# Kernel optimization log

Measured on AMD Instinct MI355X. Metric: run time of the kernel, lower is better.

## Reference

```python
import jax, jax.numpy as jnp
import numpy as np

N_NODES = 100000


def _gcn_layer(h, W, b, src, dst, norm, n):
    # h: [N, Fin] -> transform then normalized scatter-add aggregation
    h = h @ W                                   # [N, Fout]
    msg = h[src] * norm[:, None]                # [E', Fout] gather + scale
    out = jax.ops.segment_sum(msg, dst, num_segments=n)  # scatter-add
    return out + b


def setup_inputs() -> dict:
    key = jax.random.key(0)
    k1, k2, k3, k4 = jax.random.split(key, 4)
    N, F_IN, HID, C, E = N_NODES, 512, 128, 40, 1600000
    x = jax.random.normal(k1, (N, F_IN), dtype=jnp.float32)
    edge_index = jax.random.randint(k2, (2, E), 0, N, dtype=jnp.int64)
    W1 = jax.random.normal(k3, (F_IN, HID), dtype=jnp.float32) * (1.0 / np.sqrt(F_IN))
    b1 = jnp.zeros((HID,), dtype=jnp.float32)
    W2 = jax.random.normal(k4, (HID, C), dtype=jnp.float32) * (1.0 / np.sqrt(HID))
    b2 = jnp.zeros((C,), dtype=jnp.float32)
    return {"x": x, "edge_index": edge_index, "W1": W1, "b1": b1, "W2": W2, "b2": b2}


def reference(x, edge_index, W1, b1, W2, b2):
    n = x.shape[0]
    # add self-loops (GCNConv default)
    loop = jnp.arange(n, dtype=edge_index.dtype)
    src = jnp.concatenate([edge_index[0], loop])
    dst = jnp.concatenate([edge_index[1], loop])
    # symmetric normalization: deg counted on destination (in-degree, incl. self-loop)
    deg = jax.ops.segment_sum(jnp.ones_like(dst, dtype=x.dtype), dst, num_segments=n)
    dis = jnp.where(deg > 0, jax.lax.rsqrt(deg), 0.0)  # deg^{-1/2}
    norm = dis[src] * dis[dst]                          # per-edge weight

    h = jax.nn.relu(_gcn_layer(x, W1, b1, src, dst, norm, n))
    # dropout: identity in eval mode (training=False)
    h = _gcn_layer(h, W2, b2, src, dst, norm, n)
    return jax.nn.log_softmax(h, axis=1)
```

## Files before the change

### kernel.cpp

```cpp
#include <hip/hip_runtime.h>
#include <hip/hip_bf16.h>


#define F_IN 512
#define HID  128
#define NC   40

typedef __attribute__((ext_vector_type(8))) short bf16x8;
typedef __attribute__((ext_vector_type(4))) float f32x4v;

__device__ __forceinline__ ushort f2bf(float f) {
    union { float f; unsigned u; } x; x.f = f;
    unsigned r = x.u + 0x7FFFu + ((x.u >> 16) & 1u);
    return (ushort)(r >> 16);
}
__device__ __forceinline__ float bf2f(ushort u) {
    return __uint_as_float((unsigned)u << 16);
}
__device__ __forceinline__ bf16x8 cvt8(float4 lo, float4 hi) {
    __align__(16) ushort t[8];
    t[0]=f2bf(lo.x); t[1]=f2bf(lo.y); t[2]=f2bf(lo.z); t[3]=f2bf(lo.w);
    t[4]=f2bf(hi.x); t[5]=f2bf(hi.y); t[6]=f2bf(hi.z); t[7]=f2bf(hi.w);
    return *(const bf16x8*)t;
}

__global__ void count_deg(const int* __restrict__ dst, int E, unsigned* __restrict__ cnt) {
    int t = blockIdx.x * blockDim.x + threadIdx.x;
    if (t < E) atomicAdd(&cnt[dst[t]], 1u);
}

__global__ __launch_bounds__(1024) void scan_block(const unsigned* __restrict__ cnt,
                                                   unsigned* __restrict__ offs,
                                                   unsigned* __restrict__ bsums,
                                                   float* __restrict__ dis, int N) {
    __shared__ unsigned s[1024];
    int tid = threadIdx.x;
    int i = blockIdx.x * 1024 + tid;
    unsigned v = (i < N) ? cnt[i] : 0u;
    if (i < N) dis[i] = rsqrtf((float)v + 1.0f);
    s[tid] = v;
    __syncthreads();
    #pragma unroll
    for (int d = 1; d < 1024; d <<= 1) {
        unsigned t = (tid >= d) ? s[tid - d] : 0u;
        __syncthreads();
        s[tid] += t;
        __syncthreads();
    }
    if (i < N) offs[i] = s[tid] - v;
    if (tid == 1023) bsums[blockIdx.x] = s[1023];
}

__global__ __launch_bounds__(1024) void scan_bsums(unsigned* __restrict__ bsums, int nb) {
    __shared__ unsigned s[1024];
    int tid = threadIdx.x;
    unsigned v = (tid < nb) ? bsums[tid] : 0u;
    s[tid] = v;
    __syncthreads();
    #pragma unroll
    for (int d = 1; d < 1024; d <<= 1) {
        unsigned t = (tid >= d) ? s[tid - d] : 0u;
        __syncthreads();
        s[tid] += t;
        __syncthreads();
    }
    if (tid < nb) bsums[tid] = s[tid] - v;
}

__global__ __launch_bounds__(1024) void scan_add(unsigned* __restrict__ offs,
                                                 const unsigned* __restrict__ bsums,
                                                 int N, unsigned total) {
    int i = blockIdx.x * 1024 + threadIdx.x;
    if (i < N) offs[i] += bsums[blockIdx.x];
    if (i == 0) offs[N] = total;
}

__global__ void fill_csr(const int* __restrict__ src, const int* __restrict__ dst,
                         const unsigned* __restrict__ offs, unsigned* __restrict__ cursor,
                         int* __restrict__ col, int E) {
    int t = blockIdx.x * blockDim.x + threadIdx.x;
    if (t >= E) return;
    int s = src[t], d = dst[t];
    unsigned pos = offs[d] + atomicAdd(&cursor[d], 1u);
    col[pos] = s;
}

__global__ void packW(const float* __restrict__ W1, const float* __restrict__ W2,
                      ushort* __restrict__ W1p, ushort* __restrict__ W2p) {
    int t = blockIdx.x * 256 + threadIdx.x;
    if (t < 65536) {
        int j = t & 7, n = (t >> 3) & 127, kb = (t >> 10) & 3, s = t >> 12;
        int k = s * 32 + kb * 8 + j;
        W1p[t] = f2bf(W1[(size_t)k * HID + n]);
    } else {
        int q = t - 65536;
        if (q < 6144) {
            int j = q & 7;
            int i2 = q >> 3;
            int n = i2 % 48;
            int i3 = i2 / 48;
            int kb = i3 & 3, ks = i3 >> 2;
            int k = ks * 32 + kb * 8 + j;
            float v = (n < NC) ? W2[(size_t)k * NC + n] : 0.f;
            W2p[q] = f2bf(v);
        }
    }
}

__global__ __launch_bounds__(256) void gemm1_mfma(const float* __restrict__ A,
                                                  const ushort* __restrict__ Bp,
                                                  const float* __restrict__ dis,
                                                  ushort* __restrict__ C, int N) {
    const int tid  = threadIdx.x;
    const int wave = tid >> 6;
    const int lane = tid & 63;
    const int quad = lane >> 4;
    const int mr   = lane & 15;
    const int base = (blockIdx.x * 4 + wave) * 32;
    if (base >= N) return;
    const int r0 = base + mr;
    const int r1 = base + 16 + mr;
    const bool ok0 = r0 < N, ok1 = r1 < N;
    const float* ap0 = A + (size_t)(ok0 ? r0 : 0) * F_IN + quad * 8;
    const float* ap1 = A + (size_t)(ok1 ? r1 : 0) * F_IN + quad * 8;
    const ushort* bp = Bp + quad * 1024 + mr * 8;

    f32x4v acc0[8], acc1[8];
    #pragma unroll
    for (int t = 0; t < 8; t++) {
        acc0[t] = (f32x4v){0.f, 0.f, 0.f, 0.f};
        acc1[t] = (f32x4v){0.f, 0.f, 0.f, 0.f};
    }

    float4 av[2][4];
    #pragma unroll
    for (int b = 0; b < 2; b++) {
        av[b][0] = *(const float4*)(ap0 + b * 32);
        av[b][1] = *(const float4*)(ap0 + b * 32 + 4);
        av[b][2] = *(const float4*)(ap1 + b * 32);
        av[b][3] = *(const float4*)(ap1 + b * 32 + 4);
    }

    for (int s = 0; s < 16; s++) {
        bf16x8 fa0 = cvt8(av[s & 1][0], av[s & 1][1]);
        bf16x8 fa1 = cvt8(av[s & 1][2], av[s & 1][3]);
        if (s < 14) {
            av[s & 1][0] = *(const float4*)(ap0 + (s + 2) * 32);
            av[s & 1][1] = *(const float4*)(ap0 + (s + 2) * 32 + 4);
            av[s & 1][2] = *(const float4*)(ap1 + (s + 2) * 32);
            av[s & 1][3] = *(const float4*)(ap1 + (s + 2) * 32 + 4);
        }
        const ushort* bs = bp + s * 4096;
        #pragma unroll
        for (int t = 0; t < 8; t++) {
            bf16x8 b = *(const bf16x8*)(bs + t * 128);
            acc0[t] = __builtin_amdgcn_mfma_f32_16x16x32_bf16(fa0, b, acc0[t], 0, 0, 0);
            acc1[t] = __builtin_amdgcn_mfma_f32_16x16x32_bf16(fa1, b, acc1[t], 0, 0, 0);
        }
    }

    #pragma unroll
    for (int rr = 0; rr < 4; rr++) {
        int ra = base + quad * 4 + rr;
        if (ra < N) {
            float ds = dis[ra];
            #pragma unroll
            for (int t = 0; t < 8; t++)
                C[(size_t)ra * HID + t * 16 + mr] = f2bf(acc0[t][rr] * ds);
        }
        int rb = base + 16 + quad * 4 + rr;
        if (rb < N) {
            float ds = dis[rb];
            #pragma unroll
            for (int t = 0; t < 8; t++)
                C[(size_t)rb * HID + t * 16 + mr] = f2bf(acc1[t][rr] * ds);
        }
    }
}

__global__ __launch_bounds__(256) void agg1_k(const ushort* __restrict__ h,
                                              const int* __restrict__ col,
                                              const unsigned* __restrict__ offs,
                                              const float* __restrict__ dis,
                                              const float* __restrict__ b1,
                                              ushort* __restrict__ out, int N) {
    int node = blockIdx.x * 16 + (threadIdx.x >> 4);
    if (node >= N) return;
    int lane = threadIdx.x & 15;
    const size_t coff = (size_t)lane * 8;
    float a[8];
    {
        uint4 v = *(const uint4*)(h + (size_t)node * HID + coff);
        const ushort* u = (const ushort*)&v;
        #pragma unroll
        for (int j = 0; j < 8; j++) a[j] = bf2f(u[j]);
    }
    unsigned p0 = offs[node], p1 = offs[node + 1];
    unsigned p = p0;
    for (; p + 8 <= p1; p += 8) {
        int s0 = col[p],   s1 = col[p+1], s2 = col[p+2], s3 = col[p+3];
        int s4 = col[p+4], s5 = col[p+5], s6 = col[p+6], s7 = col[p+7];
        uint4 v0 = *(const uint4*)(h + (size_t)s0 * HID + coff);
        uint4 v1 = *(const uint4*)(h + (size_t)s1 * HID + coff);
        uint4 v2 = *(const uint4*)(h + (size_t)s2 * HID + coff);
        uint4 v3 = *(const uint4*)(h + (size_t)s3 * HID + coff);
        uint4 v4 = *(const uint4*)(h + (size_t)s4 * HID + coff);
        uint4 v5 = *(const uint4*)(h + (size_t)s5 * HID + coff);
        uint4 v6 = *(const uint4*)(h + (size_t)s6 * HID + coff);
        uint4 v7 = *(const uint4*)(h + (size_t)s7 * HID + coff);
        const ushort* u0 = (const ushort*)&v0;
        const ushort* u1 = (const ushort*)&v1;
        const ushort* u2 = (const ushort*)&v2;
        const ushort* u3 = (const ushort*)&v3;
        const ushort* u4 = (const ushort*)&v4;
        const ushort* u5 = (const ushort*)&v5;
        const ushort* u6 = (const ushort*)&v6;
        const ushort* u7 = (const ushort*)&v7;
        #pragma unroll
        for (int j = 0; j < 8; j++) {
            float t0 = bf2f(u0[j]) + bf2f(u1[j]);
            float t1 = bf2f(u2[j]) + bf2f(u3[j]);
            float t2 = bf2f(u4[j]) + bf2f(u5[j]);
            float t3 = bf2f(u6[j]) + bf2f(u7[j]);
            a[j] += (t0 + t1) + (t2 + t3);
        }
    }
    for (; p < p1; ++p) {
        int s = col[p];
        uint4 v = *(const uint4*)(h + (size_t)s * HID + coff);
        const ushort* u = (const ushort*)&v;
        #pragma unroll
        for (int j = 0; j < 8; j++) a[j] += bf2f(u[j]);
    }
    float dd = dis[node];
    float4 bb0 = *(const float4*)(b1 + lane * 8);
    float4 bb1 = *(const float4*)(b1 + lane * 8 + 4);
    const float bb[8] = {bb0.x, bb0.y, bb0.z, bb0.w, bb1.x, bb1.y, bb1.z, bb1.w};
    __align__(16) ushort o[8];
    #pragma unroll
    for (int j = 0; j < 8; j++) o[j] = f2bf(fmaxf(a[j] * dd + bb[j], 0.f));
    *(uint4*)(out + (size_t)node * HID + coff) = *(const uint4*)o;
}

__global__ __launch_bounds__(256) void gemm2_mfma(const ushort* __restrict__ A,
                                                  const ushort* __restrict__ W2p,
                                                  const float* __restrict__ dis,
                                                  ushort* __restrict__ h2, int N) {
    const int tid  = threadIdx.x;
    const int wave = tid >> 6;
    const int lane = tid & 63;
    const int quad = lane >> 4;
    const int mr   = lane & 15;
    const int base = (blockIdx.x * 4 + wave) * 32;
    if (base >= N) return;
    const int r0 = base + mr;
    const int r1 = base + 16 + mr;
    const bool ok0 = r0 < N, ok1 = r1 < N;
    const ushort* ap0 = A + (size_t)(ok0 ? r0 : 0) * HID + quad * 8;
    const ushort* ap1 = A + (size_t)(ok1 ? r1 : 0) * HID + quad * 8;
    const ushort* bp = W2p + quad * 384 + mr * 8;

    f32x4v acc0[3], acc1[3];
    #pragma unroll
    for (int t = 0; t < 3; t++) {
        acc0[t] = (f32x4v){0.f, 0.f, 0.f, 0.f};
        acc1[t] = (f32x4v){0.f, 0.f, 0.f, 0.f};
    }
    #pragma unroll
    for (int ks = 0; ks < 4; ks++) {
        bf16x8 a0 = *(const bf16x8*)(ap0 + ks * 32);
        bf16x8 a1 = *(const bf16x8*)(ap1 + ks * 32);
        #pragma unroll
        for (int t = 0; t < 3; t++) {
            bf16x8 b = *(const bf16x8*)(bp + ks * 1536 + t * 128);
            acc0[t] = __builtin_amdgcn_mfma_f32_16x16x32_bf16(a0, b, acc0[t], 0, 0, 0);
            acc1[t] = __builtin_amdgcn_mfma_f32_16x16x32_bf16(a1, b, acc1[t], 0, 0, 0);
        }
    }
    #pragma unroll
    for (int rr = 0; rr < 4; rr++) {
        int ra = base + quad * 4 + rr;
        if (ra < N) {
            float ds = dis[ra];
            #pragma unroll
            for (int t = 0; t < 3; t++) {
                int c = t * 16 + mr;
                if (c < NC) h2[(size_t)ra * NC + c] = f2bf(acc0[t][rr] * ds);
            }
        }
        int rb = base + 16 + quad * 4 + rr;
        if (rb < N) {
            float ds = dis[rb];
            #pragma unroll
            for (int t = 0; t < 3; t++) {
                int c = t * 16 + mr;
                if (c < NC) h2[(size_t)rb * NC + c] = f2bf(acc1[t][rr] * ds);
            }
        }
    }
}

__global__ __launch_bounds__(256) void agg2_ls(const ushort* __restrict__ h2,
                                               const int* __restrict__ col,
                                               const unsigned* __restrict__ offs,
                                               const float* __restrict__ dis,
                                               const float* __restrict__ b2,
                                               float* __restrict__ out, int N) {
    int node = blockIdx.x * 32 + (threadIdx.x >> 3);
    if (node >= N) return;
    int lane = threadIdx.x & 7;
    const bool act = lane < 5;
    const size_t coff = (size_t)lane * 8;
    float a[8] = {};
    if (act) {
        uint4 v = *(const uint4*)(h2 + (size_t)node * NC + coff);
        const ushort* u = (const ushort*)&v;
        #pragma unroll
        for (int j = 0; j < 8; j++) a[j] = bf2f(u[j]);
    }
    unsigned p0 = offs[node], p1 = offs[node + 1];
    unsigned p = p0;
    for (; p + 4 <= p1; p += 4) {
        int s0 = col[p], s1 = col[p + 1], s2 = col[p + 2], s3 = col[p + 3];
        if (act) {
            uint4 v0 = *(const uint4*)(h2 + (size_t)s0 * NC + coff);
            uint4 v1 = *(const uint4*)(h2 + (size_t)s1 * NC + coff);
            uint4 v2 = *(const uint4*)(h2 + (size_t)s2 * NC + coff);
            uint4 v3 = *(const uint4*)(h2 + (size_t)s3 * NC + coff);
            const ushort* u0 = (const ushort*)&v0;
            const ushort* u1 = (const ushort*)&v1;
            const ushort* u2 = (const ushort*)&v2;
            const ushort* u3 = (const ushort*)&v3;
            #pragma unroll
            for (int j = 0; j < 8; j++)
                a[j] += (bf2f(u0[j]) + bf2f(u1[j])) + (bf2f(u2[j]) + bf2f(u3[j]));
        }
    }
    for (; p < p1; ++p) {
        int s = col[p];
        if (act) {
            uint4 v = *(const uint4*)(h2 + (size_t)s * NC + coff);
            const ushort* u = (const ushort*)&v;
            #pragma unroll
            for (int j = 0; j < 8; j++) a[j] += bf2f(u[j]);
        }
    }
    float dd = dis[node];
    float l[8];
    float m = -1e30f;
    if (act) {
        #pragma unroll
        for (int j = 0; j < 8; j++) {
            l[j] = a[j] * dd + b2[lane * 8 + j];
            m = fmaxf(m, l[j]);
        }
    }
    #pragma unroll
    for (int d = 1; d < 8; d <<= 1) m = fmaxf(m, __shfl_xor(m, d, 8));
    float s = 0.f;
    if (act) {
        #pragma unroll
        for (int j = 0; j < 8; j++) s += __expf(l[j] - m);
    }
    #pragma unroll
    for (int d = 1; d < 8; d <<= 1) s += __shfl_xor(s, d, 8);
    float lse = m + __logf(s);
    if (act) {
        float* op = out + (size_t)node * NC + lane * 8;
        *(float4*)op       = make_float4(l[0]-lse, l[1]-lse, l[2]-lse, l[3]-lse);
        *(float4*)(op + 4) = make_float4(l[4]-lse, l[5]-lse, l[6]-lse, l[7]-lse);
    }
}

extern "C" void kernel_launch(void* const* d_in, const int* in_sizes, int n_in,
                              void* d_out, int out_size, void* d_ws, size_t ws_size,
                              hipStream_t stream) {
    const float* x  = (const float*)d_in[0];
    const int*   ei = (const int*)d_in[1];
    const float* W1 = (const float*)d_in[2];
    const float* b1 = (const float*)d_in[3];
    const float* W2 = (const float*)d_in[4];
    const float* b2 = (const float*)d_in[5];
    float* out = (float*)d_out;

    const int N = in_sizes[0] / F_IN;
    const int E = in_sizes[1] / 2;
    const int* src = ei;
    const int* dst = ei + E;

    char* ws = (char*)d_ws;
    size_t o = 0;
    unsigned* cnt  = (unsigned*)(ws + o); o += (size_t)N * 4;
    unsigned* cur  = (unsigned*)(ws + o); o += (size_t)N * 4;
    float*    dis  = (float*)   (ws + o); o += (size_t)N * 4;
    unsigned* offs = (unsigned*)(ws + o); o += (size_t)(N + 4) * 4;
    unsigned* bsums= (unsigned*)(ws + o); o += 4096;
    int*      col  = (int*)     (ws + o); o += (size_t)E * 4;
    o = (o + 15) & ~(size_t)15;
    ushort*   W1p  = (ushort*)  (ws + o); o += (size_t)F_IN * HID * 2;
    o = (o + 15) & ~(size_t)15;
    ushort*   W2p  = (ushort*)  (ws + o); o += 6144 * 2;
    o = (o + 15) & ~(size_t)15;
    ushort*   h1   = (ushort*)  (ws + o); o += (size_t)N * HID * 2;
    o = (o + 15) & ~(size_t)15;
    ushort*   ag1  = (ushort*)  (ws + o); o += (size_t)N * HID * 2;
    o = (o + 15) & ~(size_t)15;
    ushort*   h2   = (ushort*)  (ws + o); o += (size_t)N * NC * 2;

    const int nb = (N + 1023) / 1024;

    hipMemsetAsync(cnt, 0, (size_t)N * 8, stream);
    count_deg<<<(E + 255) / 256, 256, 0, stream>>>(dst, E, cnt);
    scan_block<<<nb, 1024, 0, stream>>>(cnt, offs, bsums, dis, N);
    scan_bsums<<<1, 1024, 0, stream>>>(bsums, nb);
    scan_add<<<nb, 1024, 0, stream>>>(offs, bsums, N, (unsigned)E);
    fill_csr<<<(E + 255) / 256, 256, 0, stream>>>(src, dst, offs, cur, col, E);

    packW<<<(65536 + 6144 + 255) / 256, 256, 0, stream>>>(W1, W2, W1p, W2p);

    gemm1_mfma<<<(N + 127) / 128, 256, 0, stream>>>(x, W1p, dis, h1, N);
    agg1_k<<<(N + 15) / 16, 256, 0, stream>>>(h1, col, offs, dis, b1, ag1, N);

    gemm2_mfma<<<(N + 127) / 128, 256, 0, stream>>>(ag1, W2p, dis, h2, N);
    agg2_ls<<<(N + 31) / 32, 256, 0, stream>>>(h2, col, offs, dis, b2, out, N);
}
```

Measured before the change: 601.2 us.

## Fuse prep kernels, use wave-shuffle scan, vectorize CSR index loads in aggregations

Merges degree counting and weight packing into one launch and replaces the three-kernel shared-memory scan with a wave-shuffle block scan plus a per-block prefix sum of block totals, removing two launches and many barriers. The aggregation kernels now align to 4-element boundaries and load column indices as int4 with one-step prefetch. agg2 is unrolled to 8 neighbors per iteration. This adds more peeling code paths and some register pressure.

```diff
diff --git a/kernel.cpp b/kernel.cpp
--- a/kernel.cpp
+++ b/kernel.cpp
@@ -24,70 +24,17 @@
     return *(const bf16x8*)t;
 }
 
-__global__ void count_deg(const int* __restrict__ dst, int E, unsigned* __restrict__ cnt) {
-    int t = blockIdx.x * blockDim.x + threadIdx.x;
-    if (t < E) atomicAdd(&cnt[dst[t]], 1u);
-}
-
-__global__ __launch_bounds__(1024) void scan_block(const unsigned* __restrict__ cnt,
-                                                   unsigned* __restrict__ offs,
-                                                   unsigned* __restrict__ bsums,
-                                                   float* __restrict__ dis, int N) {
-    __shared__ unsigned s[1024];
-    int tid = threadIdx.x;
-    int i = blockIdx.x * 1024 + tid;
-    unsigned v = (i < N) ? cnt[i] : 0u;
-    if (i < N) dis[i] = rsqrtf((float)v + 1.0f);
-    s[tid] = v;
-    __syncthreads();
-    #pragma unroll
-    for (int d = 1; d < 1024; d <<= 1) {
-        unsigned t = (tid >= d) ? s[tid - d] : 0u;
-        __syncthreads();
-        s[tid] += t;
-        __syncthreads();
-    }
-    if (i < N) offs[i] = s[tid] - v;
-    if (tid == 1023) bsums[blockIdx.x] = s[1023];
-}
-
-__global__ __launch_bounds__(1024) void scan_bsums(unsigned* __restrict__ bsums, int nb) {
-    __shared__ unsigned s[1024];
-    int tid = threadIdx.x;
-    unsigned v = (tid < nb) ? bsums[tid] : 0u;
-    s[tid] = v;
-    __syncthreads();
-    #pragma unroll
-    for (int d = 1; d < 1024; d <<= 1) {
-        unsigned t = (tid >= d) ? s[tid - d] : 0u;
-        __syncthreads();
-        s[tid] += t;
-        __syncthreads();
-    }
-    if (tid < nb) bsums[tid] = s[tid] - v;
-}
-
-__global__ __launch_bounds__(1024) void scan_add(unsigned* __restrict__ offs,
-                                                 const unsigned* __restrict__ bsums,
-                                                 int N, unsigned total) {
-    int i = blockIdx.x * 1024 + threadIdx.x;
-    if (i < N) offs[i] += bsums[blockIdx.x];
-    if (i == 0) offs[N] = total;
-}
-
-__global__ void fill_csr(const int* __restrict__ src, const int* __restrict__ dst,
-                         const unsigned* __restrict__ offs, unsigned* __restrict__ cursor,
-                         int* __restrict__ col, int E) {
-    int t = blockIdx.x * blockDim.x + threadIdx.x;
-    if (t >= E) return;
-    int s = src[t], d = dst[t];
-    unsigned pos = offs[d] + atomicAdd(&cursor[d], 1u);
-    col[pos] = s;
-}
-
-__global__ void packW(const float* __restrict__ W1, const float* __restrict__ W2,
-                      ushort* __restrict__ W1p, ushort* __restrict__ W2p) {
-    int t = blockIdx.x * 256 + threadIdx.x;
+__global__ void prep_k(const int* __restrict__ dst, int E, int EB,
+                       unsigned* __restrict__ cnt,
+                       const float* __restrict__ W1, const float* __restrict__ W2,
+                       ushort* __restrict__ W1p, ushort* __restrict__ W2p) {
+    int b = blockIdx.x;
+    if (b < EB) {
+        int t = b * 256 + threadIdx.x;
+        if (t < E) atomicAdd(&cnt[dst[t]], 1u);
+        return;
+    }
+    int t = (b - EB) * 256 + threadIdx.x;
     if (t < 65536) {
         int j = t & 7, n = (t >> 3) & 127, kb = (t >> 10) & 3, s = t >> 12;
         int k = s * 32 + kb * 8 + j;
@@ -105,6 +52,55 @@
             W2p[q] = f2bf(v);
         }
     }
+}
+
+__global__ __launch_bounds__(1024) void scan_block(const unsigned* __restrict__ cnt,
+                                                   unsigned* __restrict__ offs,
+                                                   unsigned* __restrict__ bsums,
+                                                   float* __restrict__ dis, int N) {
+    int tid = threadIdx.x;
+    int i = blockIdx.x * 1024 + tid;
+    unsigned v = (i < N) ? cnt[i] : 0u;
+    if (i < N) dis[i] = rsqrtf((float)v + 1.0f);
+    int lane = tid & 63, w = tid >> 6;
+    unsigned s = v;
+    #pragma unroll
+    for (int d = 1; d < 64; d <<= 1) {
+        unsigned t = __shfl_up(s, d, 64);
+        if (lane >= d) s += t;
+    }
+    __shared__ unsigned wt[16];
+    if (lane == 63) wt[w] = s;
+    __syncthreads();
+    unsigned add = 0;
+    #pragma unroll
+    for (int j = 0; j < 16; j++) add += (j < w) ? wt[j] : 0u;
+    unsigned incl = s + add;
+    if (i < N) offs[i] = incl - v;
+    if (tid == 1023) bsums[blockIdx.x] = incl;
+}
+
+__global__ __launch_bounds__(1024) void scan_add2(unsigned* __restrict__ offs,
+                                                  const unsigned* __restrict__ bsums,
+                                                  int N, unsigned total) {
+    int i = blockIdx.x * 1024 + threadIdx.x;
+    int lane = threadIdx.x & 63;
+    unsigned s = 0;
+    for (int j = lane; j < (int)blockIdx.x; j += 64) s += bsums[j];
+    #pragma unroll
+    for (int d = 1; d < 64; d <<= 1) s += __shfl_xor(s, d, 64);
+    if (i < N) offs[i] += s;
+    if (i == 0) offs[N] = total;
+}
+
+__global__ void fill_csr(const int* __restrict__ src, const int* __restrict__ dst,
+                         const unsigned* __restrict__ offs, unsigned* __restrict__ cursor,
+                         int* __restrict__ col, int E) {
+    int t = blockIdx.x * blockDim.x + threadIdx.x;
+    if (t >= E) return;
+    int s = src[t], d = dst[t];
+    unsigned pos = offs[d] + atomicAdd(&cursor[d], 1u);
+    col[pos] = s;
 }
 
 __global__ __launch_bounds__(256) void gemm1_mfma(const float* __restrict__ A,
@@ -187,27 +183,38 @@
     int node = blockIdx.x * 16 + (threadIdx.x >> 4);
     if (node >= N) return;
     int lane = threadIdx.x & 15;
-    const size_t coff = (size_t)lane * 8;
+    const ushort* hb = h + (size_t)lane * 8;
     float a[8];
     {
-        uint4 v = *(const uint4*)(h + (size_t)node * HID + coff);
+        uint4 v = *(const uint4*)(hb + (size_t)node * HID);
         const ushort* u = (const ushort*)&v;
         #pragma unroll
         for (int j = 0; j < 8; j++) a[j] = bf2f(u[j]);
     }
     unsigned p0 = offs[node], p1 = offs[node + 1];
     unsigned p = p0;
-    for (; p + 8 <= p1; p += 8) {
-        int s0 = col[p],   s1 = col[p+1], s2 = col[p+2], s3 = col[p+3];
-        int s4 = col[p+4], s5 = col[p+5], s6 = col[p+6], s7 = col[p+7];
-        uint4 v0 = *(const uint4*)(h + (size_t)s0 * HID + coff);
-        uint4 v1 = *(const uint4*)(h + (size_t)s1 * HID + coff);
-        uint4 v2 = *(const uint4*)(h + (size_t)s2 * HID + coff);
-        uint4 v3 = *(const uint4*)(h + (size_t)s3 * HID + coff);
-        uint4 v4 = *(const uint4*)(h + (size_t)s4 * HID + coff);
-        uint4 v5 = *(const uint4*)(h + (size_t)s5 * HID + coff);
-        uint4 v6 = *(const uint4*)(h + (size_t)s6 * HID + coff);
-        uint4 v7 = *(const uint4*)(h + (size_t)s7 * HID + coff);
+    while (p < p1 && (p & 3u)) {
+        int s = col[p++];
+        uint4 v = *(const uint4*)(hb + (size_t)s * HID);
+        const ushort* u = (const ushort*)&v;
+        #pragma unroll
+        for (int j = 0; j < 8; j++) a[j] += bf2f(u[j]);
+    }
+    unsigned rem = p1 - p;
+    const int4* cp = (const int4*)(col + p);
+    unsigned nb8 = rem >> 3;
+    int4 c0, c1;
+    if (nb8) { c0 = cp[0]; c1 = cp[1]; }
+    for (unsigned b = 0; b < nb8; b++) {
+        uint4 v0 = *(const uint4*)(hb + (size_t)c0.x * HID);
+        uint4 v1 = *(const uint4*)(hb + (size_t)c0.y * HID);
+        uint4 v2 = *(const uint4*)(hb + (size_t)c0.z * HID);
+        uint4 v3 = *(const uint4*)(hb + (size_t)c0.w * HID);
+        uint4 v4 = *(const uint4*)(hb + (size_t)c1.x * HID);
+        uint4 v5 = *(const uint4*)(hb + (size_t)c1.y * HID);
+        uint4 v6 = *(const uint4*)(hb + (size_t)c1.z * HID);
+        uint4 v7 = *(const uint4*)(hb + (size_t)c1.w * HID);
+        if (b + 1 < nb8) { c0 = cp[2 * b + 2]; c1 = cp[2 * b + 3]; }
         const ushort* u0 = (const ushort*)&v0;
         const ushort* u1 = (const ushort*)&v1;
         const ushort* u2 = (const ushort*)&v2;
@@ -225,9 +232,25 @@
             a[j] += (t0 + t1) + (t2 + t3);
         }
     }
+    p += nb8 << 3;
+    if (rem & 4u) {
+        int4 c = *(const int4*)(col + p);
+        uint4 v0 = *(const uint4*)(hb + (size_t)c.x * HID);
+        uint4 v1 = *(const uint4*)(hb + (size_t)c.y * HID);
+        uint4 v2 = *(const uint4*)(hb + (size_t)c.z * HID);
+        uint4 v3 = *(const uint4*)(hb + (size_t)c.w * HID);
+        const ushort* u0 = (const ushort*)&v0;
+        const ushort* u1 = (const ushort*)&v1;
+        const ushort* u2 = (const ushort*)&v2;
+        const ushort* u3 = (const ushort*)&v3;
+        #pragma unroll
+        for (int j = 0; j < 8; j++)
+            a[j] += (bf2f(u0[j]) + bf2f(u1[j])) + (bf2f(u2[j]) + bf2f(u3[j]));
+        p += 4;
+    }
     for (; p < p1; ++p) {
         int s = col[p];
-        uint4 v = *(const uint4*)(h + (size_t)s * HID + coff);
+        uint4 v = *(const uint4*)(hb + (size_t)s * HID);
         const ushort* u = (const ushort*)&v;
         #pragma unroll
         for (int j = 0; j < 8; j++) a[j] += bf2f(u[j]);
@@ -239,7 +262,7 @@
     __align__(16) ushort o[8];
     #pragma unroll
     for (int j = 0; j < 8; j++) o[j] = f2bf(fmaxf(a[j] * dd + bb[j], 0.f));
-    *(uint4*)(out + (size_t)node * HID + coff) = *(const uint4*)o;
+    *(uint4*)(out + (size_t)node * HID + (size_t)lane * 8) = *(const uint4*)o;
 }
 
 __global__ __launch_bounds__(256) void gemm2_mfma(const ushort* __restrict__ A,
@@ -310,36 +333,83 @@
     if (node >= N) return;
     int lane = threadIdx.x & 7;
     const bool act = lane < 5;
-    const size_t coff = (size_t)lane * 8;
+    const ushort* hb = h2 + (size_t)lane * 8;
     float a[8] = {};
     if (act) {
-        uint4 v = *(const uint4*)(h2 + (size_t)node * NC + coff);
+        uint4 v = *(const uint4*)(hb + (size_t)node * NC);
         const ushort* u = (const ushort*)&v;
         #pragma unroll
         for (int j = 0; j < 8; j++) a[j] = bf2f(u[j]);
     }
     unsigned p0 = offs[node], p1 = offs[node + 1];
     unsigned p = p0;
-    for (; p + 4 <= p1; p += 4) {
-        int s0 = col[p], s1 = col[p + 1], s2 = col[p + 2], s3 = col[p + 3];
+    while (p < p1 && (p & 3u)) {
+        int s = col[p++];
         if (act) {
-            uint4 v0 = *(const uint4*)(h2 + (size_t)s0 * NC + coff);
-            uint4 v1 = *(const uint4*)(h2 + (size_t)s1 * NC + coff);
-            uint4 v2 = *(const uint4*)(h2 + (size_t)s2 * NC + coff);
-            uint4 v3 = *(const uint4*)(h2 + (size_t)s3 * NC + coff);
+            uint4 v = *(const uint4*)(hb + (size_t)s * NC);
+            const ushort* u = (const ushort*)&v;
+            #pragma unroll
+            for (int j = 0; j < 8; j++) a[j] += bf2f(u[j]);
+        }
+    }
+    unsigned rem = p1 - p;
+    const int4* cp = (const int4*)(col + p);
+    unsigned nb8 = rem >> 3;
+    int4 c0, c1;
+    if (nb8) { c0 = cp[0]; c1 = cp[1]; }
+    for (unsigned b = 0; b < nb8; b++) {
+        int s0 = c0.x, s1 = c0.y, s2 = c0.z, s3 = c0.w;
+        int s4 = c1.x, s5 = c1.y, s6 = c1.z, s7 = c1.w;
+        if (b + 1 < nb8) { c0 = cp[2 * b + 2]; c1 = cp[2 * b + 3]; }
+        if (act) {
+            uint4 v0 = *(const uint4*)(hb + (size_t)s0 * NC);
+            uint4 v1 = *(const uint4*)(hb + (size_t)s1 * NC);
+            uint4 v2 = *(const uint4*)(hb + (size_t)s2 * NC);
+            uint4 v3 = *(const uint4*)(hb + (size_t)s3 * NC);
+            uint4 v4 = *(const uint4*)(hb + (size_t)s4 * NC);
+            uint4 v5 = *(const uint4*)(hb + (size_t)s5 * NC);
+            uint4 v6 = *(const uint4*)(hb + (size_t)s6 * NC);
+            uint4 v7 = *(const uint4*)(hb + (size_t)s7 * NC);
             const ushort* u0 = (const ushort*)&v0;
             const ushort* u1 = (const ushort*)&v1;
             const ushort* u2 = (const ushort*)&v2;
             const ushort* u3 = (const ushort*)&v3;
+            const ushort* u4 = (const ushort*)&v4;
+            const ushort* u5 = (const ushort*)&v5;
+            const ushort* u6 = (const ushort*)&v6;
+            const ushort* u7 = (const ushort*)&v7;
+            #pragma unroll
+            for (int j = 0; j < 8; j++) {
+                float t0 = bf2f(u0[j]) + bf2f(u1[j]);
+                float t1 = bf2f(u2[j]) + bf2f(u3[j]);
+                float t2 = bf2f(u4[j]) + bf2f(u5[j]);
+                float t3 = bf2f(u6[j]) + bf2f(u7[j]);
+                a[j] += (t0 + t1) + (t2 + t3);
+            }
+        }
+    }
+    p += nb8 << 3;
+    if (rem & 4u) {
+        int4 c = *(const int4*)(col + p);
+        if (act) {
+            uint4 v0 = *(const uint4*)(hb + (size_t)c.x * NC);
+            uint4 v1 = *(const uint4*)(hb + (size_t)c.y * NC);
+            uint4 v2 = *(const uint4*)(hb + (size_t)c.z * NC);
+            uint4 v3 = *(const uint4*)(hb + (size_t)c.w * NC);
+            const ushort* u0 = (const ushort*)&v0;
+            const ushort* u1 = (const ushort*)&v1;
+            const ushort* u2 = (const ushort*)&v2;
+            const ushort* u3 = (const ushort*)&v3;
             #pragma unroll
             for (int j = 0; j < 8; j++)
                 a[j] += (bf2f(u0[j]) + bf2f(u1[j])) + (bf2f(u2[j]) + bf2f(u3[j]));
         }
+        p += 4;
     }
     for (; p < p1; ++p) {
         int s = col[p];
         if (act) {
-            uint4 v = *(const uint4*)(h2 + (size_t)s * NC + coff);
+            uint4 v = *(const uint4*)(hb + (size_t)s * NC);
             const ushort* u = (const ushort*)&v;
             #pragma unroll
             for (int j = 0; j < 8; j++) a[j] += bf2f(u[j]);
@@ -408,15 +478,14 @@
     ushort*   h2   = (ushort*)  (ws + o); o += (size_t)N * NC * 2;
 
     const int nb = (N + 1023) / 1024;
+    const int EB = (E + 255) / 256;
+    const int PB = (65536 + 6144 + 255) / 256;
 
     hipMemsetAsync(cnt, 0, (size_t)N * 8, stream);
-    count_deg<<<(E + 255) / 256, 256, 0, stream>>>(dst, E, cnt);
+    prep_k<<<EB + PB, 256, 0, stream>>>(dst, E, EB, cnt, W1, W2, W1p, W2p);
     scan_block<<<nb, 1024, 0, stream>>>(cnt, offs, bsums, dis, N);
-    scan_bsums<<<1, 1024, 0, stream>>>(bsums, nb);
-    scan_add<<<nb, 1024, 0, stream>>>(offs, bsums, N, (unsigned)E);
+    scan_add2<<<nb, 1024, 0, stream>>>(offs, bsums, N, (unsigned)E);
     fill_csr<<<(E + 255) / 256, 256, 0, stream>>>(src, dst, offs, cur, col, E);
-
-    packW<<<(65536 + 6144 + 255) / 256, 256, 0, stream>>>(W1, W2, W1p, W2p);
 
     gemm1_mfma<<<(N + 127) / 128, 256, 0, stream>>>(x, W1p, dis, h1, N);
     agg1_k<<<(N + 15) / 16, 256, 0, stream>>>(h1, col, offs, dis, b1, ag1, N);
```

Result: no change. 597.4 us (-0.6%).
